# Kernel optimization log

Measured on AMD Instinct MI355X. Metric: run time of the kernel, lower is better.

Reference implementation:

```python
import jax, jax.numpy as jnp
import numpy as np

NUM_HEADS = 16
FUTURE_FRAMES = 2
DIM = 1024


def setup_inputs() -> dict:
    key = jax.random.key(0)
    kx, kqkv, kp, kb = jax.random.split(key, 4)
    B, T = 2, 2048
    x = jax.random.normal(kx, (B, T, DIM), dtype=jnp.float32)
    # torch Linear weights stored transposed for direct x @ W use
    w_qkv = jax.random.normal(kqkv, (DIM, 3 * DIM), dtype=jnp.float32) * (DIM ** -0.5)
    w_proj = jax.random.normal(kp, (DIM, DIM), dtype=jnp.float32) * (DIM ** -0.5)
    b_proj = jax.random.normal(kb, (DIM,), dtype=jnp.float32) * 0.01
    return {"x": x, "w_qkv": w_qkv, "w_proj": w_proj, "b_proj": b_proj}


def reference(x, w_qkv, w_proj, b_proj):
    B, T, dim = x.shape
    H = NUM_HEADS
    hd = dim // H
    qkv = x @ w_qkv                                    # (B, T, 3*dim)
    q, k, v = jnp.split(qkv, 3, axis=-1)
    # (B, H, T, hd)
    q = q.reshape(B, T, H, hd).transpose(0, 2, 1, 3)
    k = k.reshape(B, T, H, hd).transpose(0, 2, 1, 3)
    v = v.reshape(B, T, H, hd).transpose(0, 2, 1, 3)
    scale = hd ** -0.5
    scores = jnp.einsum('bhqd,bhkd->bhqk', q, k) * scale
    # banded mask: query i may attend keys j with i <= j <= i + future_frames
    i = jnp.arange(T)[:, None]
    j = jnp.arange(T)[None, :]
    allowed = (j >= i) & (j <= i + FUTURE_FRAMES)       # (T, T)
    scores = jnp.where(allowed[None, None], scores, -jnp.inf)
    attn = jax.nn.softmax(scores, axis=-1)
    out = jnp.einsum('bhqk,bhkd->bhqd', attn, v)        # (B, H, T, hd)
    out = out.transpose(0, 2, 1, 3).reshape(B, T, dim)
    return out @ w_proj + b_proj
```

## Files before the change

### kernel.cpp

```cpp
#include <hip/hip_runtime.h>
#include <hip/hip_bf16.h>
#include <cstdint>
#include <cstddef>

#define T_SEQ 2048
#define NBATCH 2
#define DIMSZ 1024
#define NHEAD 16
#define HDIM 64

typedef float f32x4 __attribute__((ext_vector_type(4)));
typedef short bf16x8 __attribute__((ext_vector_type(8)));

__device__ __forceinline__ void gld_lds16(const __hip_bfloat16* g, __hip_bfloat16* l) {
    __builtin_amdgcn_global_load_lds(
        (const __attribute__((address_space(1))) unsigned int*)g,
        (__attribute__((address_space(3))) unsigned int*)l,
        16, 0, 0);
}

__global__ __launch_bounds__(256) void prep(
    const float* __restrict__ x,      __hip_bfloat16* __restrict__ xb,
    const float* __restrict__ wqkv,   __hip_bfloat16* __restrict__ wqkvT,
    const float* __restrict__ wproj,  __hip_bfloat16* __restrict__ wprojT)
{
    __shared__ float tile[32][33];
    const int b = blockIdx.x;
    if (b < 4096) {
        int i = (b * 256 + threadIdx.x) * 4;
        float4 v = *(const float4*)(x + i);
        union { __hip_bfloat16 h[4]; ushort4 u; } pk;
        pk.h[0] = __hip_bfloat16(v.x); pk.h[1] = __hip_bfloat16(v.y);
        pk.h[2] = __hip_bfloat16(v.z); pk.h[3] = __hip_bfloat16(v.w);
        *(ushort4*)(xb + i) = pk.u;
        return;
    }
    const float* in; __hip_bfloat16* out; int R, C, c0, r0;
    if (b < 7168) {
        int bb = b - 4096; in = wqkv; out = wqkvT; R = 1024; C = 3072;
        c0 = (bb % 96) * 32; r0 = (bb / 96) * 32;
    } else {
        int bb = b - 7168; in = wproj; out = wprojT; R = 1024; C = 1024;
        c0 = (bb & 31) * 32; r0 = (bb >> 5) * 32;
    }
    const int tx = threadIdx.x & 31, ty = threadIdx.x >> 5;
#pragma unroll
    for (int p = 0; p < 32; p += 8)
        tile[ty + p][tx] = in[(size_t)(r0 + ty + p) * C + c0 + tx];
    __syncthreads();
#pragma unroll
    for (int p = 0; p < 32; p += 8)
        out[(size_t)(c0 + ty + p) * R + r0 + tx] = __hip_bfloat16(tile[tx][ty + p]);
}

__global__ __launch_bounds__(256) void gemm_bt_128(
    const __hip_bfloat16* __restrict__ A,
    const __hip_bfloat16* __restrict__ Bt,
    __hip_bfloat16* __restrict__ C,
    int M, int N, int K)
{
    __shared__ __align__(16) __hip_bfloat16 As[128 * 32];
    __shared__ __align__(16) __hip_bfloat16 Bs[128 * 32];

    const int tid  = threadIdx.x;
    const int wv   = tid >> 6;
    const int lane = tid & 63;
    const int bn   = blockIdx.x, bm = blockIdx.y;
    const int wm   = wv >> 1, wn = wv & 1;

    f32x4 acc[4][4] = {};

    const int srow = lane >> 2;
    const int scol = (lane & 3) * 8;

    const __hip_bfloat16* Ag = A  + (size_t)(bm * 128) * K;
    const __hip_bfloat16* Bg = Bt + (size_t)(bn * 128) * K;

    const int fm = lane & 15;
    const int fq = (lane >> 4) * 8;

    for (int kk = 0; kk < K; kk += 32) {
#pragma unroll
        for (int it = 0; it < 2; ++it) {
            int row = (it * 4 + wv) * 16 + srow;
            gld_lds16(Ag + (size_t)row * K + kk + scol, As + row * 32 + scol);
            gld_lds16(Bg + (size_t)row * K + kk + scol, Bs + row * 32 + scol);
        }
        __syncthreads();

        bf16x8 af[4], bfr[4];
#pragma unroll
        for (int i = 0; i < 4; ++i)
            af[i] = *(const bf16x8*)(As + (wm * 64 + i * 16 + fm) * 32 + fq);
#pragma unroll
        for (int j = 0; j < 4; ++j)
            bfr[j] = *(const bf16x8*)(Bs + (wn * 64 + j * 16 + fm) * 32 + fq);

#pragma unroll
        for (int i = 0; i < 4; ++i)
#pragma unroll
            for (int j = 0; j < 4; ++j)
                acc[i][j] = __builtin_amdgcn_mfma_f32_16x16x32_bf16(af[i], bfr[j], acc[i][j], 0, 0, 0);
        __syncthreads();
    }

    const int fcol  = lane & 15;
    const int frow4 = (lane >> 4) * 4;
    const int cm0 = bm * 128 + wm * 64;
    const int cn0 = bn * 128 + wn * 64;
#pragma unroll
    for (int j = 0; j < 4; ++j) {
        int col = cn0 + j * 16 + fcol;
#pragma unroll
        for (int i = 0; i < 4; ++i)
#pragma unroll
            for (int r = 0; r < 4; ++r) {
                int row = cm0 + i * 16 + frow4 + r;
                C[(size_t)row * N + col] = __hip_bfloat16(acc[i][j][r]);
            }
    }
}

__global__ __launch_bounds__(256) void gemm_bt_64(
    const __hip_bfloat16* __restrict__ A,
    const __hip_bfloat16* __restrict__ Bt,
    const float* __restrict__ bias,
    float* __restrict__ C,
    int M, int N, int K)
{
    __shared__ __align__(16) __hip_bfloat16 As[64 * 32];
    __shared__ __align__(16) __hip_bfloat16 Bs[128 * 32];

    const int tid  = threadIdx.x;
    const int wv   = tid >> 6;
    const int lane = tid & 63;
    const int bn   = blockIdx.x, bm = blockIdx.y;
    const int wm   = wv >> 1, wn = wv & 1;

    f32x4 acc[2][4] = {};

    const int srow = lane >> 2;
    const int scol = (lane & 3) * 8;

    const __hip_bfloat16* Ag = A  + (size_t)(bm * 64) * K;
    const __hip_bfloat16* Bg = Bt + (size_t)(bn * 128) * K;

    const int fm = lane & 15;
    const int fq = (lane >> 4) * 8;

    for (int kk = 0; kk < K; kk += 32) {
        {
            int row = wv * 16 + srow;
            gld_lds16(Ag + (size_t)row * K + kk + scol, As + row * 32 + scol);
        }
#pragma unroll
        for (int it = 0; it < 2; ++it) {
            int row = (it * 4 + wv) * 16 + srow;
            gld_lds16(Bg + (size_t)row * K + kk + scol, Bs + row * 32 + scol);
        }
        __syncthreads();

        bf16x8 af[2], bfr[4];
#pragma unroll
        for (int i = 0; i < 2; ++i)
            af[i] = *(const bf16x8*)(As + (wm * 32 + i * 16 + fm) * 32 + fq);
#pragma unroll
        for (int j = 0; j < 4; ++j)
            bfr[j] = *(const bf16x8*)(Bs + (wn * 64 + j * 16 + fm) * 32 + fq);

#pragma unroll
        for (int i = 0; i < 2; ++i)
#pragma unroll
            for (int j = 0; j < 4; ++j)
                acc[i][j] = __builtin_amdgcn_mfma_f32_16x16x32_bf16(af[i], bfr[j], acc[i][j], 0, 0, 0);
        __syncthreads();
    }

    const int fcol  = lane & 15;
    const int frow4 = (lane >> 4) * 4;
    const int cm0 = bm * 64 + wm * 32;
    const int cn0 = bn * 128 + wn * 64;
#pragma unroll
    for (int j = 0; j < 4; ++j) {
        int col = cn0 + j * 16 + fcol;
        float bv = bias[col];
#pragma unroll
        for (int i = 0; i < 2; ++i)
#pragma unroll
            for (int r = 0; r < 4; ++r) {
                int row = cm0 + i * 16 + frow4 + r;
                C[(size_t)row * N + col] = acc[i][j][r] + bv;
            }
    }
}

__global__ __launch_bounds__(256) void attn_banded(
    const __hip_bfloat16* __restrict__ qkv,
    __hip_bfloat16* __restrict__ o)
{
    const int lane = threadIdx.x & 63;
    const int wid  = blockIdx.x * 4 + (threadIdx.x >> 6);
    const int h = wid & (NHEAD - 1);
    const int r = wid >> 4;
    const int t = r & (T_SEQ - 1);
    const size_t rb = (size_t)r * (3 * DIMSZ);
    const int hc = h * HDIM + lane;

    float q = (float)qkv[rb + hc];
    float s[3], vv[3];
#pragma unroll
    for (int j = 0; j < 3; ++j) {
        bool ok = (t + j) < T_SEQ;
        size_t rbj = ok ? rb + (size_t)j * (3 * DIMSZ) : rb;
        float kj = (float)qkv[rbj + DIMSZ + hc];
        vv[j]    = (float)qkv[rbj + 2 * DIMSZ + hc];
        float d = q * kj;
#pragma unroll
        for (int off = 32; off > 0; off >>= 1)
            d += __shfl_xor(d, off, 64);
        s[j] = ok ? d * 0.125f : -1e30f;
    }
    float m = fmaxf(s[0], fmaxf(s[1], s[2]));
    float p0 = __expf(s[0] - m), p1 = __expf(s[1] - m), p2 = __expf(s[2] - m);
    float inv = 1.0f / (p0 + p1 + p2);
    float out = (p0 * vv[0] + p1 * vv[1] + p2 * vv[2]) * inv;
    o[(size_t)r * DIMSZ + hc] = __hip_bfloat16(out);
}

extern "C" void kernel_launch(void* const* d_in, const int* in_sizes, int n_in,
                              void* d_out, int out_size, void* d_ws, size_t ws_size,
                              hipStream_t stream) {
    const float* x      = (const float*)d_in[0];
    const float* w_qkv  = (const float*)d_in[1];
    const float* w_proj = (const float*)d_in[2];
    const float* b_proj = (const float*)d_in[3];
    float* out = (float*)d_out;

    const int M = NBATCH * T_SEQ;

    char* ws = (char*)d_ws;
    __hip_bfloat16* xb     = (__hip_bfloat16*)(ws);
    __hip_bfloat16* attn   = (__hip_bfloat16*)(ws);
    __hip_bfloat16* wqkvT  = (__hip_bfloat16*)(ws + (8u  << 20));
    __hip_bfloat16* wprojT = (__hip_bfloat16*)(ws + (14u << 20));
    __hip_bfloat16* qkv    = (__hip_bfloat16*)(ws + (16u << 20));

    prep<<<8192, 256, 0, stream>>>(x, xb, w_qkv, wqkvT, w_proj, wprojT);

    gemm_bt_128<<<dim3(3 * DIMSZ / 128, M / 128), 256, 0, stream>>>(
        xb, wqkvT, qkv, M, 3 * DIMSZ, DIMSZ);

    attn_banded<<<M * NHEAD / 4, 256, 0, stream>>>(qkv, attn);

    gemm_bt_64<<<dim3(DIMSZ / 128, M / 64), 256, 0, stream>>>(
        attn, wprojT, b_proj, out, M, DIMSZ, DIMSZ);
}
```

Measured before the change: 154.4 us.

## Double K-step per barrier in GEMMs and vectorize banded attention per row

```diff
diff --git a/kernel.cpp b/kernel.cpp
--- a/kernel.cpp
+++ b/kernel.cpp
@@ -17,6 +17,10 @@
         (const __attribute__((address_space(1))) unsigned int*)g,
         (__attribute__((address_space(3))) unsigned int*)l,
         16, 0, 0);
+}
+
+__device__ __forceinline__ float bf2f(unsigned short u) {
+    union { unsigned int i; float f; } c; c.i = (unsigned int)u << 16; return c.f;
 }
 
 __global__ __launch_bounds__(256) void prep(
@@ -59,8 +63,8 @@
     __hip_bfloat16* __restrict__ C,
     int M, int N, int K)
 {
-    __shared__ __align__(16) __hip_bfloat16 As[128 * 32];
-    __shared__ __align__(16) __hip_bfloat16 Bs[128 * 32];
+    __shared__ __align__(16) __hip_bfloat16 As[2 * 128 * 32];
+    __shared__ __align__(16) __hip_bfloat16 Bs[2 * 128 * 32];
 
     const int tid  = threadIdx.x;
     const int wv   = tid >> 6;
@@ -79,28 +83,34 @@
     const int fm = lane & 15;
     const int fq = (lane >> 4) * 8;
 
-    for (int kk = 0; kk < K; kk += 32) {
-#pragma unroll
-        for (int it = 0; it < 2; ++it) {
-            int row = (it * 4 + wv) * 16 + srow;
-            gld_lds16(Ag + (size_t)row * K + kk + scol, As + row * 32 + scol);
-            gld_lds16(Bg + (size_t)row * K + kk + scol, Bs + row * 32 + scol);
+    for (int kk = 0; kk < K; kk += 64) {
+#pragma unroll
+        for (int kh = 0; kh < 2; ++kh)
+#pragma unroll
+            for (int it = 0; it < 2; ++it) {
+                int row = (it * 4 + wv) * 16 + srow;
+                gld_lds16(Ag + (size_t)row * K + kk + kh * 32 + scol,
+                          As + kh * 4096 + row * 32 + scol);
+                gld_lds16(Bg + (size_t)row * K + kk + kh * 32 + scol,
+                          Bs + kh * 4096 + row * 32 + scol);
+            }
+        __syncthreads();
+
+#pragma unroll
+        for (int kh = 0; kh < 2; ++kh) {
+            bf16x8 af[4], bfr[4];
+#pragma unroll
+            for (int i = 0; i < 4; ++i)
+                af[i] = *(const bf16x8*)(As + kh * 4096 + (wm * 64 + i * 16 + fm) * 32 + fq);
+#pragma unroll
+            for (int j = 0; j < 4; ++j)
+                bfr[j] = *(const bf16x8*)(Bs + kh * 4096 + (wn * 64 + j * 16 + fm) * 32 + fq);
+#pragma unroll
+            for (int i = 0; i < 4; ++i)
+#pragma unroll
+                for (int j = 0; j < 4; ++j)
+                    acc[i][j] = __builtin_amdgcn_mfma_f32_16x16x32_bf16(af[i], bfr[j], acc[i][j], 0, 0, 0);
         }
-        __syncthreads();
-
-        bf16x8 af[4], bfr[4];
-#pragma unroll
-        for (int i = 0; i < 4; ++i)
-            af[i] = *(const bf16x8*)(As + (wm * 64 + i * 16 + fm) * 32 + fq);
-#pragma unroll
-        for (int j = 0; j < 4; ++j)
-            bfr[j] = *(const bf16x8*)(Bs + (wn * 64 + j * 16 + fm) * 32 + fq);
-
-#pragma unroll
-        for (int i = 0; i < 4; ++i)
-#pragma unroll
-            for (int j = 0; j < 4; ++j)
-                acc[i][j] = __builtin_amdgcn_mfma_f32_16x16x32_bf16(af[i], bfr[j], acc[i][j], 0, 0, 0);
         __syncthreads();
     }
 
@@ -128,8 +138,8 @@
     float* __restrict__ C,
     int M, int N, int K)
 {
-    __shared__ __align__(16) __hip_bfloat16 As[64 * 32];
-    __shared__ __align__(16) __hip_bfloat16 Bs[128 * 32];
+    __shared__ __align__(16) __hip_bfloat16 As[2 * 64 * 32];
+    __shared__ __align__(16) __hip_bfloat16 Bs[2 * 128 * 32];
 
     const int tid  = threadIdx.x;
     const int wv   = tid >> 6;
@@ -148,31 +158,38 @@
     const int fm = lane & 15;
     const int fq = (lane >> 4) * 8;
 
-    for (int kk = 0; kk < K; kk += 32) {
-        {
-            int row = wv * 16 + srow;
-            gld_lds16(Ag + (size_t)row * K + kk + scol, As + row * 32 + scol);
+    for (int kk = 0; kk < K; kk += 64) {
+#pragma unroll
+        for (int kh = 0; kh < 2; ++kh) {
+            {
+                int row = wv * 16 + srow;
+                gld_lds16(Ag + (size_t)row * K + kk + kh * 32 + scol,
+                          As + kh * 2048 + row * 32 + scol);
+            }
+#pragma unroll
+            for (int it = 0; it < 2; ++it) {
+                int row = (it * 4 + wv) * 16 + srow;
+                gld_lds16(Bg + (size_t)row * K + kk + kh * 32 + scol,
+                          Bs + kh * 4096 + row * 32 + scol);
+            }
         }
-#pragma unroll
-        for (int it = 0; it < 2; ++it) {
-            int row = (it * 4 + wv) * 16 + srow;
-            gld_lds16(Bg + (size_t)row * K + kk + scol, Bs + row * 32 + scol);
+        __syncthreads();
+
+#pragma unroll
+        for (int kh = 0; kh < 2; ++kh) {
+            bf16x8 af[2], bfr[4];
+#pragma unroll
+            for (int i = 0; i < 2; ++i)
+                af[i] = *(const bf16x8*)(As + kh * 2048 + (wm * 32 + i * 16 + fm) * 32 + fq);
+#pragma unroll
+            for (int j = 0; j < 4; ++j)
+                bfr[j] = *(const bf16x8*)(Bs + kh * 4096 + (wn * 64 + j * 16 + fm) * 32 + fq);
+#pragma unroll
+            for (int i = 0; i < 2; ++i)
+#pragma unroll
+                for (int j = 0; j < 4; ++j)
+                    acc[i][j] = __builtin_amdgcn_mfma_f32_16x16x32_bf16(af[i], bfr[j], acc[i][j], 0, 0, 0);
         }
-        __syncthreads();
-
-        bf16x8 af[2], bfr[4];
-#pragma unroll
-        for (int i = 0; i < 2; ++i)
-            af[i] = *(const bf16x8*)(As + (wm * 32 + i * 16 + fm) * 32 + fq);
-#pragma unroll
-        for (int j = 0; j < 4; ++j)
-            bfr[j] = *(const bf16x8*)(Bs + (wn * 64 + j * 16 + fm) * 32 + fq);
-
-#pragma unroll
-        for (int i = 0; i < 2; ++i)
-#pragma unroll
-            for (int j = 0; j < 4; ++j)
-                acc[i][j] = __builtin_amdgcn_mfma_f32_16x16x32_bf16(af[i], bfr[j], acc[i][j], 0, 0, 0);
         __syncthreads();
     }
 
@@ -198,33 +215,39 @@
     const __hip_bfloat16* __restrict__ qkv,
     __hip_bfloat16* __restrict__ o)
 {
-    const int lane = threadIdx.x & 63;
-    const int wid  = blockIdx.x * 4 + (threadIdx.x >> 6);
-    const int h = wid & (NHEAD - 1);
-    const int r = wid >> 4;
-    const int t = r & (T_SEQ - 1);
+    const int t4 = threadIdx.x;
+    const int r  = blockIdx.x;
+    const int t  = r & (T_SEQ - 1);
     const size_t rb = (size_t)r * (3 * DIMSZ);
-    const int hc = h * HDIM + lane;
-
-    float q = (float)qkv[rb + hc];
-    float s[3], vv[3];
+    const int d0 = t4 * 4;
+
+    ushort4 qu = *(const ushort4*)(qkv + rb + d0);
+    float q0 = bf2f(qu.x), q1 = bf2f(qu.y), q2 = bf2f(qu.z), q3 = bf2f(qu.w);
+
+    float s[3];
+    float vvx[3], vvy[3], vvz[3], vvw[3];
 #pragma unroll
     for (int j = 0; j < 3; ++j) {
         bool ok = (t + j) < T_SEQ;
         size_t rbj = ok ? rb + (size_t)j * (3 * DIMSZ) : rb;
-        float kj = (float)qkv[rbj + DIMSZ + hc];
-        vv[j]    = (float)qkv[rbj + 2 * DIMSZ + hc];
-        float d = q * kj;
-#pragma unroll
-        for (int off = 32; off > 0; off >>= 1)
+        ushort4 ku = *(const ushort4*)(qkv + rbj + DIMSZ + d0);
+        ushort4 vu = *(const ushort4*)(qkv + rbj + 2 * DIMSZ + d0);
+        vvx[j] = bf2f(vu.x); vvy[j] = bf2f(vu.y); vvz[j] = bf2f(vu.z); vvw[j] = bf2f(vu.w);
+        float d = q0 * bf2f(ku.x) + q1 * bf2f(ku.y) + q2 * bf2f(ku.z) + q3 * bf2f(ku.w);
+#pragma unroll
+        for (int off = 8; off > 0; off >>= 1)
             d += __shfl_xor(d, off, 64);
         s[j] = ok ? d * 0.125f : -1e30f;
     }
-    float m = fmaxf(s[0], fmaxf(s[1], s[2]));
+    float m  = fmaxf(s[0], fmaxf(s[1], s[2]));
     float p0 = __expf(s[0] - m), p1 = __expf(s[1] - m), p2 = __expf(s[2] - m);
     float inv = 1.0f / (p0 + p1 + p2);
-    float out = (p0 * vv[0] + p1 * vv[1] + p2 * vv[2]) * inv;
-    o[(size_t)r * DIMSZ + hc] = __hip_bfloat16(out);
+    union { __hip_bfloat16 h[4]; ushort4 u; } pk;
+    pk.h[0] = __hip_bfloat16((p0 * vvx[0] + p1 * vvx[1] + p2 * vvx[2]) * inv);
+    pk.h[1] = __hip_bfloat16((p0 * vvy[0] + p1 * vvy[1] + p2 * vvy[2]) * inv);
+    pk.h[2] = __hip_bfloat16((p0 * vvz[0] + p1 * vvz[1] + p2 * vvz[2]) * inv);
+    pk.h[3] = __hip_bfloat16((p0 * vvw[0] + p1 * vvw[1] + p2 * vvw[2]) * inv);
+    *(ushort4*)(o + (size_t)r * DIMSZ + d0) = pk.u;
 }
 
 extern "C" void kernel_launch(void* const* d_in, const int* in_sizes, int n_in,
@@ -250,7 +273,7 @@
     gemm_bt_128<<<dim3(3 * DIMSZ / 128, M / 128), 256, 0, stream>>>(
         xb, wqkvT, qkv, M, 3 * DIMSZ, DIMSZ);
 
-    attn_banded<<<M * NHEAD / 4, 256, 0, stream>>>(qkv, attn);
+    attn_banded<<<M, 256, 0, stream>>>(qkv, attn);
 
     gemm_bt_64<<<dim3(DIMSZ / 128, M / 64), 256, 0, stream>>>(
         attn, wprojT, b_proj, out, M, DIMSZ, DIMSZ);
```

After: 145.2 us. 1.06x faster.
